# Performance work log

Measured on AMD Instinct MI355X. Metric: run time of the kernel, lower is better.

## Reference

```python
import jax, jax.numpy as jnp
import numpy as np

GAMMA = 1.0

def setup_inputs() -> dict:
    key = jax.random.key(0)
    k1, k2 = jax.random.split(key)
    source_features = jax.random.normal(k1, (4096, 2048), dtype=jnp.float32)
    target_features = jax.random.normal(k2, (4096, 2048), dtype=jnp.float32)
    return {"source_features": source_features, "target_features": target_features}

def _gaussian_kernel_mean(x, y, gamma):
    # Original: ((x_i - y_j)**2).mean(-1) / D  == sqdist_ij / D**2
    # Computed via the x^2 + y^2 - 2xy GEMM trick instead of tiling O(N*M*D).
    d = x.shape[1]
    x2 = jnp.sum(x * x, axis=1)  # [N]
    y2 = jnp.sum(y * y, axis=1)  # [M]
    xy = x @ y.T                 # [N, M]
    sqdist = x2[:, None] + y2[None, :] - 2.0 * xy
    k = jnp.exp(-gamma * sqdist / (d * d))
    return jnp.mean(k)

def reference(source_features, target_features):
    source = source_features.reshape(source_features.shape[0], -1)
    target = target_features.reshape(target_features.shape[0], -1)
    # Equal batch sizes -> padding branch in the original is a no-op.
    xx = _gaussian_kernel_mean(source, source, GAMMA)
    yy = _gaussian_kernel_mean(target, target, GAMMA)
    xy = _gaussian_kernel_mean(source, target, GAMMA)
    return xx + yy - 2.0 * xy
```

## Files before the change

kernel.cpp:

```cpp
#include <hip/hip_runtime.h>
#include <stdint.h>
#include <stddef.h>

#define AS1 __attribute__((address_space(1)))
#define AS3 __attribute__((address_space(3)))

typedef short bf16x8 __attribute__((ext_vector_type(8)));
typedef float f32x4 __attribute__((ext_vector_type(4)));
typedef unsigned short u16x8 __attribute__((ext_vector_type(8)));

static constexpr int N = 4096;
static constexpr int K = 2048;
static constexpr int BM = 128;
static constexpr int TILES = N / BM;
static constexpr int NBLK = TILES * TILES;

__device__ __forceinline__ unsigned short f2bf(float f) {
  union { float f; uint32_t u; } v; v.f = f;
  return (unsigned short)((v.u + 0x7FFFu + ((v.u >> 16) & 1u)) >> 16);
}

__global__ __launch_bounds__(256) void prep_kernel(
    const float* __restrict__ X, const float* __restrict__ Y,
    float* __restrict__ x2, float* __restrict__ y2,
    unsigned short* __restrict__ Xb, unsigned short* __restrict__ Yb, int wb) {
  const int row = blockIdx.x;
  const float* src = blockIdx.y ? Y : X;
  float* nrm = blockIdx.y ? y2 : x2;
  unsigned short* dst = blockIdx.y ? Yb : Xb;
  const size_t base = (size_t)row * K + threadIdx.x * 8;
  const float4 a = *(const float4*)(src + base);
  const float4 b = *(const float4*)(src + base + 4);
  double s = (double)a.x * a.x + (double)a.y * a.y + (double)a.z * a.z +
             (double)a.w * a.w + (double)b.x * b.x + (double)b.y * b.y +
             (double)b.z * b.z + (double)b.w * b.w;
  if (wb) {
    u16x8 o;
    o[0] = f2bf(a.x); o[1] = f2bf(a.y); o[2] = f2bf(a.z); o[3] = f2bf(a.w);
    o[4] = f2bf(b.x); o[5] = f2bf(b.y); o[6] = f2bf(b.z); o[7] = f2bf(b.w);
    *(u16x8*)(dst + base) = o;
  }
#pragma unroll
  for (int off = 32; off; off >>= 1) s += __shfl_down(s, off);
  __shared__ double red[4];
  if ((threadIdx.x & 63) == 0) red[threadIdx.x >> 6] = s;
  __syncthreads();
  if (threadIdx.x == 0) nrm[row] = (float)(red[0] + red[1] + red[2] + red[3]);
}


#define RB3(bb, o) ((unsigned)((bb)*32768u + (o)*16384u))
#define VM2 asm volatile("s_waitcnt vmcnt(2)" ::: "memory")
#define VM_NONE

#define STG(O, TT, BB, H)                                                      \
  do {                                                                         \
    const unsigned short* _sp = (O) ? Bpan : Apan;                             \
    const unsigned int _so =                                                   \
        ((O) ? sB : sA) + (unsigned)(H) * 262144u + (unsigned)(TT) * 64u;      \
    const unsigned int _lb = RB3(BB, O) + (unsigned)(H) * 8192u + wseg;        \
    __builtin_amdgcn_global_load_lds(                                          \
        (const AS1 unsigned int*)(_sp + _so),                                  \
        (AS3 unsigned int*)(lds + _lb), 16, 0, 0);                             \
    __builtin_amdgcn_global_load_lds(                                          \
        (const AS1 unsigned int*)(_sp + _so + 16384u),                         \
        (AS3 unsigned int*)(lds + _lb + 512u), 16, 0, 0);                      \
  } while (0)

#define PH(KS, NH, BB, VMW, ...)                                               \
  do {                                                                         \
    if constexpr ((NH) == 0) {                                                 \
      _Pragma("unroll") for (int _mi = 0; _mi < 8; ++_mi)                      \
          af[_mi] = *(const bf16x8*)(lds + RB3(BB, 0) +                        \
                                     (aoff[_mi] ^ ((KS) * 32u)));              \
    }                                                                          \
    bf16x8 _b0 = *(const bf16x8*)(lds + RB3(BB, 1) +                           \
                                  (boff[(NH) * 2] ^ ((KS) * 32u)));            \
    bf16x8 _b1 = *(const bf16x8*)(lds + RB3(BB, 1) +                           \
                                  (boff[(NH) * 2 + 1] ^ ((KS) * 32u)));        \
    __VA_ARGS__;                                                               \
    __builtin_amdgcn_s_barrier();                                              \
    __builtin_amdgcn_s_setprio(1);                                             \
    _Pragma("unroll") for (int _mi = 0; _mi < 8; ++_mi) {                      \
      acc[_mi][(NH) * 2] = __builtin_amdgcn_mfma_f32_16x16x32_bf16(            \
          af[_mi], _b0, acc[_mi][(NH) * 2], 0, 0, 0);                          \
      acc[_mi][(NH) * 2 + 1] = __builtin_amdgcn_mfma_f32_16x16x32_bf16(        \
          af[_mi], _b1, acc[_mi][(NH) * 2 + 1], 0, 0, 0);                      \
    }                                                                          \
    __builtin_amdgcn_s_setprio(0);                                             \
    VMW;                                                                       \
    __builtin_amdgcn_s_barrier();                                              \
  } while (0)

#define TILE3(T, BB)                                                           \
  do {                                                                         \
    const int _t1 = ((T) + 1 < 32) ? (T) + 1 : 31;                             \
    const int _t2 = ((T) + 2 < 32) ? (T) + 2 : 31;                             \
    PH(0, 0, BB, VM_NONE, STG(0, _t1, 1 - (BB), 1));                           \
    PH(0, 1, BB, VM_NONE, STG(1, _t1, 1 - (BB), 0));                           \
    PH(1, 0, BB, VM_NONE, STG(1, _t1, 1 - (BB), 1));                           \
    PH(1, 1, BB, VM2,     STG(0, _t2, (BB), 0));                               \
  } while (0)

__global__ __launch_bounds__(512, 2) void mmd_gemm8(
    const unsigned short* __restrict__ Xb, const unsigned short* __restrict__ Yb,
    const float* __restrict__ x2, const float* __restrict__ y2,
    double* __restrict__ partials) {
  __shared__ __align__(16) unsigned short lds[65536];

  const int bid = blockIdx.x;
  const int logical = (bid & 7) * 62 + (bid >> 3);
  int ti, tj;
  const unsigned short *Apan, *Bpan;
  const float *rn, *cn;
  double wgt;
  if (logical < 256) {
    ti = logical & 15; tj = logical >> 4;
    Apan = Xb; Bpan = Yb; rn = x2; cn = y2; wgt = -2.0;
  } else {
    const int q = logical - 256;
    const int pp = q / 120;
    int jj = q % 120;
    int rr = 0;
    while (jj >= 15 - rr) { jj -= 15 - rr; ++rr; }
    ti = rr; tj = rr + 1 + jj;
    Apan = Bpan = pp ? Yb : Xb;
    rn = cn = pp ? y2 : x2;
    wgt = 2.0;
  }
  const int i0 = ti << 8, j0 = tj << 8;

  const int tid = threadIdx.x;
  const int w = tid >> 6, l = tid & 63;
  const int wm = w >> 2, wn = w & 3;
  const int lr = l & 15, lq = l >> 4;

  const int ci = w * 128 + l;
  const int rr0 = ci >> 3;
  const int cc0 = (ci & 7) ^ (rr0 & 7);
  const unsigned int sA = (unsigned)(i0 + rr0) * (unsigned)K + (unsigned)(cc0 * 8);
  const unsigned int sB = (unsigned)(j0 + rr0) * (unsigned)K + (unsigned)(cc0 * 8);
  const unsigned int wseg = (unsigned)w * 1024u;

  unsigned int aoff[8], boff[4];
#pragma unroll
  for (int mi = 0; mi < 8; ++mi) {
    const int r = wm * 128 + mi * 16 + lr;
    aoff[mi] = (unsigned)(r * 64 + ((lq ^ (r & 7)) * 8));
  }
#pragma unroll
  for (int ni = 0; ni < 4; ++ni) {
    const int rb = wn * 64 + ni * 16 + lr;
    boff[ni] = (unsigned)(rb * 64 + ((lq ^ (rb & 7)) * 8));
  }

  f32x4 acc[8][4] = {};
  bf16x8 af[8];

  STG(0, 0, 0, 0); STG(0, 0, 0, 1); STG(1, 0, 0, 0); STG(1, 0, 0, 1);
  STG(0, 1, 1, 0);
  VM2;
  __builtin_amdgcn_s_barrier();

#pragma unroll 1
  for (int tt = 0; tt < 32; tt += 2) {
    TILE3(tt, 0);
    TILE3(tt + 1, 1);
  }

  const float ce = -1.0f / (2048.0f * 2048.0f);
  double s = 0.0;
#pragma unroll
  for (int mi = 0; mi < 8; ++mi) {
#pragma unroll
    for (int r4 = 0; r4 < 4; ++r4) {
      const float rv = rn[i0 + wm * 128 + mi * 16 + lq * 4 + r4];
#pragma unroll
      for (int ni = 0; ni < 4; ++ni) {
        const float cv = cn[j0 + wn * 64 + ni * 16 + lr];
        const float tx = ce * (rv + cv - 2.0f * acc[mi][ni][r4]);
        const float v =
            tx * (1.0f + tx * (0.5f + tx * (0.16666667f + tx * 0.041666668f)));
        s += (double)v;
      }
    }
  }
#pragma unroll
  for (int off = 32; off; off >>= 1) s += __shfl_down(s, off);
  __shared__ double red[8];
  if (l == 0) red[w] = s;
  __syncthreads();
  if (tid == 0) {
    double tot = 0.0;
#pragma unroll
    for (int i = 0; i < 8; ++i) tot += red[i];
    partials[logical] = wgt * tot;
  }
}

__global__ __launch_bounds__(256) void mmd_sym128(
    const unsigned short* __restrict__ Xb, const unsigned short* __restrict__ Yb,
    const float* __restrict__ x2, const float* __restrict__ y2,
    double* __restrict__ partials) {
  const int bid = blockIdx.x;
  const int logical = (bid & 7) * 12 + (bid >> 3);
  const int p = logical / 48;
  const int r2_ = logical % 48;
  const int d = r2_ / 3;
  const int sub = r2_ % 3;
  const double wgt = (sub == 1) ? 2.0 : 1.0;

  const unsigned short* Pan = p ? Yb : Xb;
  const float* nrm = p ? y2 : x2;
  const int i0 = d * 256 + ((sub == 2) ? 128 : 0);
  const int j0 = d * 256 + ((sub >= 1) ? 128 : 0);

  __shared__ __align__(16) unsigned short As[128 * 64];
  __shared__ __align__(16) unsigned short Bs[128 * 64];

  const int tid = threadIdx.x;
  const int w = tid >> 6, l = tid & 63;
  const int m_base = (w >> 1) * 64, n_base = (w & 1) * 64;
  const int lr = l & 15, lq = l >> 4;

  f32x4 acc[4][4] = {};

  for (int k0 = 0; k0 < K; k0 += 64) {
#pragma unroll
    for (int u = 0; u < 4; ++u) {
      const int seg = w * 4 + u;
      const int f = seg * 64 + l;
      const int row = f >> 3;
      const int scol = ((f & 7) ^ (row & 7)) * 8;
      __builtin_amdgcn_global_load_lds(
          (const AS1 unsigned int*)(Pan + (size_t)(i0 + row) * K + k0 + scol),
          (AS3 unsigned int*)(As + seg * 512), 16, 0, 0);
      __builtin_amdgcn_global_load_lds(
          (const AS1 unsigned int*)(Pan + (size_t)(j0 + row) * K + k0 + scol),
          (AS3 unsigned int*)(Bs + seg * 512), 16, 0, 0);
    }
    __syncthreads();

#pragma unroll
    for (int kk = 0; kk < 64; kk += 32) {
      bf16x8 af2[4], bfr[4];
      const int ch = (kk >> 3) + lq;
#pragma unroll
      for (int mi = 0; mi < 4; ++mi) {
        const int r = m_base + mi * 16 + lr;
        af2[mi] = *(const bf16x8*)((const char*)As + r * 128 + ((ch ^ (r & 7)) * 16));
      }
#pragma unroll
      for (int ni = 0; ni < 4; ++ni) {
        const int r = n_base + ni * 16 + lr;
        bfr[ni] = *(const bf16x8*)((const char*)Bs + r * 128 + ((ch ^ (r & 7)) * 16));
      }
#pragma unroll
      for (int mi = 0; mi < 4; ++mi)
#pragma unroll
        for (int ni = 0; ni < 4; ++ni)
          acc[mi][ni] = __builtin_amdgcn_mfma_f32_16x16x32_bf16(
              af2[mi], bfr[ni], acc[mi][ni], 0, 0, 0);
    }
    __syncthreads();
  }

  const float ce = -1.0f / (2048.0f * 2048.0f);
  double s = 0.0;
#pragma unroll
  for (int mi = 0; mi < 4; ++mi) {
#pragma unroll
    for (int r4 = 0; r4 < 4; ++r4) {
      const float rv = nrm[i0 + m_base + mi * 16 + lq * 4 + r4];
#pragma unroll
      for (int ni = 0; ni < 4; ++ni) {
        const float cv = nrm[j0 + n_base + ni * 16 + lr];
        const float tx = ce * (rv + cv - 2.0f * acc[mi][ni][r4]);
        const float v =
            tx * (1.0f + tx * (0.5f + tx * (0.16666667f + tx * 0.041666668f)));
        s += (double)v;
      }
    }
  }
#pragma unroll
  for (int off = 32; off; off >>= 1) s += __shfl_down(s, off);
  __shared__ double red[4];
  if (l == 0) red[w] = s;
  __syncthreads();
  if (tid == 0)
    partials[496 + logical] = wgt * (red[0] + red[1] + red[2] + red[3]);
}

__global__ __launch_bounds__(256) void mmd_gemm_f32(
    const float* __restrict__ Xp, const float* __restrict__ Yp,
    const float* __restrict__ x2, const float* __restrict__ y2,
    double* __restrict__ partials) {
  const int p = blockIdx.y;
  const float* Ap = (p == 1) ? Yp : Xp;
  const float* Bp = (p == 0) ? Xp : Yp;
  const float* rn = (p == 1) ? y2 : x2;
  const float* cn = (p == 0) ? x2 : y2;
  const double wgt = (p == 2) ? -2.0 : 1.0;

  const int bx = blockIdx.x;
  const int i0 = (bx & (TILES - 1)) * BM;
  const int j0 = (bx / TILES) * BM;

  __shared__ __align__(16) unsigned short As[BM * 64];
  __shared__ __align__(16) unsigned short Bs[BM * 64];

  const int tid = threadIdx.x;
  const int w = tid >> 6, l = tid & 63;
  const int m_base = (w >> 1) * 64, n_base = (w & 1) * 64;

  f32x4 acc[4][4] = {};

  for (int k0 = 0; k0 < K; k0 += 64) {
#pragma unroll
    for (int u = 0; u < 4; ++u) {
      const int f = u * 256 + tid;
      const int row = f >> 3;
      const int cir = f & 7;
      const int dstb = row * 128 + ((cir ^ (row & 7)) * 16);
      {
        const float* g = Ap + (size_t)(i0 + row) * K + k0 + cir * 8;
        const float4 v0 = *(const float4*)g;
        const float4 v1 = *(const float4*)(g + 4);
        u16x8 o;
        o[0] = f2bf(v0.x); o[1] = f2bf(v0.y); o[2] = f2bf(v0.z); o[3] = f2bf(v0.w);
        o[4] = f2bf(v1.x); o[5] = f2bf(v1.y); o[6] = f2bf(v1.z); o[7] = f2bf(v1.w);
        *(u16x8*)((char*)As + dstb) = o;
      }
      {
        const float* g = Bp + (size_t)(j0 + row) * K + k0 + cir * 8;
        const float4 v0 = *(const float4*)g;
        const float4 v1 = *(const float4*)(g + 4);
        u16x8 o;
        o[0] = f2bf(v0.x); o[1] = f2bf(v0.y); o[2] = f2bf(v0.z); o[3] = f2bf(v0.w);
        o[4] = f2bf(v1.x); o[5] = f2bf(v1.y); o[6] = f2bf(v1.z); o[7] = f2bf(v1.w);
        *(u16x8*)((char*)Bs + dstb) = o;
      }
    }
    __syncthreads();

#pragma unroll
    for (int kk = 0; kk < 64; kk += 32) {
      bf16x8 af2[4], bfr[4];
      const int lr = l & 15;
      const int ch = (kk >> 3) + (l >> 4);
#pragma unroll
      for (int mi = 0; mi < 4; ++mi) {
        const int r = m_base + mi * 16 + lr;
        af2[mi] = *(const bf16x8*)((const char*)As + r * 128 + ((ch ^ (r & 7)) * 16));
      }
#pragma unroll
      for (int ni = 0; ni < 4; ++ni) {
        const int r = n_base + ni * 16 + lr;
        bfr[ni] = *(const bf16x8*)((const char*)Bs + r * 128 + ((ch ^ (r & 7)) * 16));
      }
#pragma unroll
      for (int mi = 0; mi < 4; ++mi)
#pragma unroll
        for (int ni = 0; ni < 4; ++ni)
          acc[mi][ni] = __builtin_amdgcn_mfma_f32_16x16x32_bf16(
              af2[mi], bfr[ni], acc[mi][ni], 0, 0, 0);
    }
    __syncthreads();
  }

  const float ce = -1.0f / (2048.0f * 2048.0f);
  double s = 0.0;
  const int lr = l & 15, lq = l >> 4;
#pragma unroll
  for (int mi = 0; mi < 4; ++mi) {
#pragma unroll
    for (int r4 = 0; r4 < 4; ++r4) {
      const float rv = rn[i0 + m_base + mi * 16 + lq * 4 + r4];
#pragma unroll
      for (int ni = 0; ni < 4; ++ni) {
        const float cv = cn[j0 + n_base + ni * 16 + lr];
        const float tx = ce * (rv + cv - 2.0f * acc[mi][ni][r4]);
        const float v =
            tx * (1.0f + tx * (0.5f + tx * (0.16666667f + tx * 0.041666668f)));
        s += (double)v;
      }
    }
  }
#pragma unroll
  for (int off = 32; off; off >>= 1) s += __shfl_down(s, off);
  __shared__ double red[4];
  if (l == 0) red[w] = s;
  __syncthreads();
  if (tid == 0) partials[p * NBLK + bx] = wgt * (red[0] + red[1] + red[2] + red[3]);
}

__global__ __launch_bounds__(256) void finalize_kernel(
    const double* __restrict__ partials, float* __restrict__ out, int n) {
  double s = 0.0;
  for (int i = threadIdx.x; i < n; i += 256) s += partials[i];
#pragma unroll
  for (int off = 32; off; off >>= 1) s += __shfl_down(s, off);
  __shared__ double red[4];
  if ((threadIdx.x & 63) == 0) red[threadIdx.x >> 6] = s;
  __syncthreads();
  if (threadIdx.x == 0)
    out[0] = (float)((red[0] + red[1] + red[2] + red[3]) *
                     (1.0 / ((double)N * (double)N)));
}

extern "C" void kernel_launch(void* const* d_in, const int* in_sizes, int n_in,
                              void* d_out, int out_size, void* d_ws,
                              size_t ws_size, hipStream_t stream) {
  const float* X = (const float*)d_in[0];
  const float* Y = (const float*)d_in[1];
  char* ws = (char*)d_ws;

  double* partials = (double*)ws;
  float* x2 = (float*)(ws + 24576);
  float* y2 = (float*)(ws + 24576 + 16384);
  unsigned short* Xb = (unsigned short*)(ws + 65536);
  unsigned short* Yb = Xb + (size_t)N * K;
  const size_t need_fast = (size_t)65536 + (size_t)2 * N * K * 2;
  const bool fast = ws_size >= need_fast;

  prep_kernel<<<dim3(N, 2), 256, 0, stream>>>(X, Y, x2, y2, Xb, Yb, fast ? 1 : 0);
  if (fast) {
    mmd_gemm8<<<dim3(496), dim3(512), 0, stream>>>(Xb, Yb, x2, y2, partials);
    mmd_sym128<<<dim3(96), dim3(256), 0, stream>>>(Xb, Yb, x2, y2, partials);
    finalize_kernel<<<1, 256, 0, stream>>>(partials, (float*)d_out, 592);
  } else {
    mmd_gemm_f32<<<dim3(NBLK, 3), 256, 0, stream>>>(X, Y, x2, y2, partials);
    finalize_kernel<<<1, 256, 0, stream>>>(partials, (float*)d_out, 3072);
  }
}
```

Measured before the change: 180.1 us.

## Fold diagonal tiles into main GEMM kernel as double-work blocks, drop sym128 kernel

Removes the separate mmd_sym128 kernel that handled the diagonal 256x256 tiles with a 128-tile GEMM. The 32 diagonal tiles (16 for X·X and 16 for Y·Y) now run as the first 16 blocks of mmd_gemm8, each computing two full 256x256 tiles in sequence, and the grid grows to 512 blocks with one fewer launch. This also regroups the staging loads inside TILE3 so two loads issue in one phase and another phase issues none. The trade-off is that diagonal tiles now compute the full square instead of the upper half. The 16 double-work blocks may also lengthen the tail.

```diff
diff --git a/kernel.cpp b/kernel.cpp
--- a/kernel.cpp
+++ b/kernel.cpp
@@ -97,8 +97,8 @@
     const int _t1 = ((T) + 1 < 32) ? (T) + 1 : 31;                             \
     const int _t2 = ((T) + 2 < 32) ? (T) + 2 : 31;                             \
     PH(0, 0, BB, VM_NONE, STG(0, _t1, 1 - (BB), 1));                           \
-    PH(0, 1, BB, VM_NONE, STG(1, _t1, 1 - (BB), 0));                           \
-    PH(1, 0, BB, VM_NONE, STG(1, _t1, 1 - (BB), 1));                           \
+    PH(0, 1, BB, VM_NONE, STG(1, _t1, 1 - (BB), 0); STG(1, _t1, 1 - (BB), 1)); \
+    PH(1, 0, BB, VM_NONE, );                                                   \
     PH(1, 1, BB, VM2,     STG(0, _t2, (BB), 0));                               \
   } while (0)
 
@@ -107,28 +107,13 @@
     const float* __restrict__ x2, const float* __restrict__ y2,
     double* __restrict__ partials) {
   __shared__ __align__(16) unsigned short lds[65536];
+  __shared__ double red[8];
 
   const int bid = blockIdx.x;
-  const int logical = (bid & 7) * 62 + (bid >> 3);
-  int ti, tj;
-  const unsigned short *Apan, *Bpan;
-  const float *rn, *cn;
-  double wgt;
-  if (logical < 256) {
-    ti = logical & 15; tj = logical >> 4;
-    Apan = Xb; Bpan = Yb; rn = x2; cn = y2; wgt = -2.0;
-  } else {
-    const int q = logical - 256;
-    const int pp = q / 120;
-    int jj = q % 120;
-    int rr = 0;
-    while (jj >= 15 - rr) { jj -= 15 - rr; ++rr; }
-    ti = rr; tj = rr + 1 + jj;
-    Apan = Bpan = pp ? Yb : Xb;
-    rn = cn = pp ? y2 : x2;
-    wgt = 2.0;
-  }
-  const int i0 = ti << 8, j0 = tj << 8;
+  const bool dbl = bid < 16;
+  const int nsub = dbl ? 2 : 1;
+  int lg = 0;
+  if (!dbl) lg = ((bid - 16) & 7) * 62 + ((bid - 16) >> 3);
 
   const int tid = threadIdx.x;
   const int w = tid >> 6, l = tid & 63;
@@ -138,8 +123,6 @@
   const int ci = w * 128 + l;
   const int rr0 = ci >> 3;
   const int cc0 = (ci & 7) ^ (rr0 & 7);
-  const unsigned int sA = (unsigned)(i0 + rr0) * (unsigned)K + (unsigned)(cc0 * 8);
-  const unsigned int sB = (unsigned)(j0 + rr0) * (unsigned)K + (unsigned)(cc0 * 8);
   const unsigned int wseg = (unsigned)w * 1024u;
 
   unsigned int aoff[8], boff[4];
@@ -154,141 +137,81 @@
     boff[ni] = (unsigned)(rb * 64 + ((lq ^ (rb & 7)) * 8));
   }
 
-  f32x4 acc[8][4] = {};
-  bf16x8 af[8];
-
-  STG(0, 0, 0, 0); STG(0, 0, 0, 1); STG(1, 0, 0, 0); STG(1, 0, 0, 1);
-  STG(0, 1, 1, 0);
-  VM2;
-  __builtin_amdgcn_s_barrier();
-
 #pragma unroll 1
-  for (int tt = 0; tt < 32; tt += 2) {
-    TILE3(tt, 0);
-    TILE3(tt + 1, 1);
-  }
-
-  const float ce = -1.0f / (2048.0f * 2048.0f);
-  double s = 0.0;
-#pragma unroll
-  for (int mi = 0; mi < 8; ++mi) {
-#pragma unroll
-    for (int r4 = 0; r4 < 4; ++r4) {
-      const float rv = rn[i0 + wm * 128 + mi * 16 + lq * 4 + r4];
-#pragma unroll
-      for (int ni = 0; ni < 4; ++ni) {
-        const float cv = cn[j0 + wn * 64 + ni * 16 + lr];
-        const float tx = ce * (rv + cv - 2.0f * acc[mi][ni][r4]);
-        const float v =
-            tx * (1.0f + tx * (0.5f + tx * (0.16666667f + tx * 0.041666668f)));
-        s += (double)v;
-      }
-    }
-  }
-#pragma unroll
-  for (int off = 32; off; off >>= 1) s += __shfl_down(s, off);
-  __shared__ double red[8];
-  if (l == 0) red[w] = s;
-  __syncthreads();
-  if (tid == 0) {
-    double tot = 0.0;
-#pragma unroll
-    for (int i = 0; i < 8; ++i) tot += red[i];
-    partials[logical] = wgt * tot;
-  }
-}
-
-__global__ __launch_bounds__(256) void mmd_sym128(
-    const unsigned short* __restrict__ Xb, const unsigned short* __restrict__ Yb,
-    const float* __restrict__ x2, const float* __restrict__ y2,
-    double* __restrict__ partials) {
-  const int bid = blockIdx.x;
-  const int logical = (bid & 7) * 12 + (bid >> 3);
-  const int p = logical / 48;
-  const int r2_ = logical % 48;
-  const int d = r2_ / 3;
-  const int sub = r2_ % 3;
-  const double wgt = (sub == 1) ? 2.0 : 1.0;
-
-  const unsigned short* Pan = p ? Yb : Xb;
-  const float* nrm = p ? y2 : x2;
-  const int i0 = d * 256 + ((sub == 2) ? 128 : 0);
-  const int j0 = d * 256 + ((sub >= 1) ? 128 : 0);
-
-  __shared__ __align__(16) unsigned short As[128 * 64];
-  __shared__ __align__(16) unsigned short Bs[128 * 64];
-
-  const int tid = threadIdx.x;
-  const int w = tid >> 6, l = tid & 63;
-  const int m_base = (w >> 1) * 64, n_base = (w & 1) * 64;
-  const int lr = l & 15, lq = l >> 4;
-
-  f32x4 acc[4][4] = {};
-
-  for (int k0 = 0; k0 < K; k0 += 64) {
-#pragma unroll
-    for (int u = 0; u < 4; ++u) {
-      const int seg = w * 4 + u;
-      const int f = seg * 64 + l;
-      const int row = f >> 3;
-      const int scol = ((f & 7) ^ (row & 7)) * 8;
-      __builtin_amdgcn_global_load_lds(
-          (const AS1 unsigned int*)(Pan + (size_t)(i0 + row) * K + k0 + scol),
-          (AS3 unsigned int*)(As + seg * 512), 16, 0, 0);
-      __builtin_amdgcn_global_load_lds(
-          (const AS1 unsigned int*)(Pan + (size_t)(j0 + row) * K + k0 + scol),
-          (AS3 unsigned int*)(Bs + seg * 512), 16, 0, 0);
-    }
+  for (int sub = 0; sub < nsub; ++sub) {
+    int ti, tj, slot;
+    const unsigned short *Apan, *Bpan;
+    const float *rn, *cn;
+    double wgt;
+    if (dbl) {
+      ti = tj = bid;
+      Apan = Bpan = sub ? Yb : Xb;
+      rn = cn = sub ? y2 : x2;
+      wgt = 1.0;
+      slot = bid * 2 + sub;
+    } else if (lg < 256) {
+      ti = lg & 15; tj = lg >> 4;
+      Apan = Xb; Bpan = Yb; rn = x2; cn = y2; wgt = -2.0;
+      slot = 32 + lg;
+    } else {
+      const int q = lg - 256;
+      const int pp = q / 120;
+      int jj = q % 120;
+      int rr = 0;
+      while (jj >= 15 - rr) { jj -= 15 - rr; ++rr; }
+      ti = rr; tj = rr + 1 + jj;
+      Apan = Bpan = pp ? Yb : Xb;
+      rn = cn = pp ? y2 : x2;
+      wgt = 2.0;
+      slot = 32 + lg;
+    }
+    const int i0 = ti << 8, j0 = tj << 8;
+    const unsigned int sA = (unsigned)(i0 + rr0) * (unsigned)K + (unsigned)(cc0 * 8);
+    const unsigned int sB = (unsigned)(j0 + rr0) * (unsigned)K + (unsigned)(cc0 * 8);
+
+    f32x4 acc[8][4] = {};
+    bf16x8 af[8];
+
+    STG(0, 0, 0, 0); STG(0, 0, 0, 1); STG(1, 0, 0, 0); STG(1, 0, 0, 1);
+    STG(0, 1, 1, 0);
+    VM2;
+    __builtin_amdgcn_s_barrier();
+
+#pragma unroll 1
+    for (int tt = 0; tt < 32; tt += 2) {
+      TILE3(tt, 0);
+      TILE3(tt + 1, 1);
+    }
+
+    const float ce = -1.0f / (2048.0f * 2048.0f);
+    double s = 0.0;
+#pragma unroll
+    for (int mi = 0; mi < 8; ++mi) {
+#pragma unroll
+      for (int r4 = 0; r4 < 4; ++r4) {
+        const float rv = rn[i0 + wm * 128 + mi * 16 + lq * 4 + r4];
+#pragma unroll
+        for (int ni = 0; ni < 4; ++ni) {
+          const float cv = cn[j0 + wn * 64 + ni * 16 + lr];
+          const float tx = ce * (rv + cv - 2.0f * acc[mi][ni][r4]);
+          const float v =
+              tx * (1.0f + tx * (0.5f + tx * (0.16666667f + tx * 0.041666668f)));
+          s += (double)v;
+        }
+      }
+    }
+#pragma unroll
+    for (int off = 32; off; off >>= 1) s += __shfl_down(s, off);
+    if (l == 0) red[w] = s;
     __syncthreads();
-
-#pragma unroll
-    for (int kk = 0; kk < 64; kk += 32) {
-      bf16x8 af2[4], bfr[4];
-      const int ch = (kk >> 3) + lq;
-#pragma unroll
-      for (int mi = 0; mi < 4; ++mi) {
-        const int r = m_base + mi * 16 + lr;
-        af2[mi] = *(const bf16x8*)((const char*)As + r * 128 + ((ch ^ (r & 7)) * 16));
-      }
-#pragma unroll
-      for (int ni = 0; ni < 4; ++ni) {
-        const int r = n_base + ni * 16 + lr;
-        bfr[ni] = *(const bf16x8*)((const char*)Bs + r * 128 + ((ch ^ (r & 7)) * 16));
-      }
-#pragma unroll
-      for (int mi = 0; mi < 4; ++mi)
-#pragma unroll
-        for (int ni = 0; ni < 4; ++ni)
-          acc[mi][ni] = __builtin_amdgcn_mfma_f32_16x16x32_bf16(
-              af2[mi], bfr[ni], acc[mi][ni], 0, 0, 0);
+    if (tid == 0) {
+      double tot = 0.0;
+#pragma unroll
+      for (int i = 0; i < 8; ++i) tot += red[i];
+      partials[slot] = wgt * tot;
     }
     __syncthreads();
   }
-
-  const float ce = -1.0f / (2048.0f * 2048.0f);
-  double s = 0.0;
-#pragma unroll
-  for (int mi = 0; mi < 4; ++mi) {
-#pragma unroll
-    for (int r4 = 0; r4 < 4; ++r4) {
-      const float rv = nrm[i0 + m_base + mi * 16 + lq * 4 + r4];
-#pragma unroll
-      for (int ni = 0; ni < 4; ++ni) {
-        const float cv = nrm[j0 + n_base + ni * 16 + lr];
-        const float tx = ce * (rv + cv - 2.0f * acc[mi][ni][r4]);
-        const float v =
-            tx * (1.0f + tx * (0.5f + tx * (0.16666667f + tx * 0.041666668f)));
-        s += (double)v;
-      }
-    }
-  }
-#pragma unroll
-  for (int off = 32; off; off >>= 1) s += __shfl_down(s, off);
-  __shared__ double red[4];
-  if (l == 0) red[w] = s;
-  __syncthreads();
-  if (tid == 0)
-    partials[496 + logical] = wgt * (red[0] + red[1] + red[2] + red[3]);
 }
 
 __global__ __launch_bounds__(256) void mmd_gemm_f32(
@@ -425,9 +348,8 @@
 
   prep_kernel<<<dim3(N, 2), 256, 0, stream>>>(X, Y, x2, y2, Xb, Yb, fast ? 1 : 0);
   if (fast) {
-    mmd_gemm8<<<dim3(496), dim3(512), 0, stream>>>(Xb, Yb, x2, y2, partials);
-    mmd_sym128<<<dim3(96), dim3(256), 0, stream>>>(Xb, Yb, x2, y2, partials);
-    finalize_kernel<<<1, 256, 0, stream>>>(partials, (float*)d_out, 592);
+    mmd_gemm8<<<dim3(512), dim3(512), 0, stream>>>(Xb, Yb, x2, y2, partials);
+    finalize_kernel<<<1, 256, 0, stream>>>(partials, (float*)d_out, 528);
   } else {
     mmd_gemm_f32<<<dim3(NBLK, 3), 256, 0, stream>>>(X, Y, x2, y2, partials);
     finalize_kernel<<<1, 256, 0, stream>>>(partials, (float*)d_out, 3072);
```

After: 195.6 us. 8.6% more time.

## Prefetch LDS fragments one phase ahead and use one barrier per phase

Applied to the files above, without the earlier changes.

The GEMM main loop is software-pipelined so that the LDS reads of A and B fragments for the next phase are issued right after the current phase's MFMAs. An explicit lgkmcnt(0) wait plus a sched_barrier is placed before each MFMA group, and the second s_barrier in each phase is dropped. The goal is to hide LDS read latency behind matrix math and to halve barrier synchronization. In exchange it keeps the B fragments in extra registers. The first reads of the next buffer are also issued before the barrier, which could race with other waves' global-to-LDS loads.

```diff
diff --git a/kernel.cpp b/kernel.cpp
--- a/kernel.cpp
+++ b/kernel.cpp
@@ -51,7 +51,11 @@
 
 #define RB3(bb, o) ((unsigned)((bb)*32768u + (o)*16384u))
 #define VM2 asm volatile("s_waitcnt vmcnt(2)" ::: "memory")
-#define VM_NONE
+#define LGKM0                                                                  \
+  do {                                                                         \
+    asm volatile("s_waitcnt lgkmcnt(0)" ::: "memory");                         \
+    __builtin_amdgcn_sched_barrier(0);                                         \
+  } while (0)
 
 #define STG(O, TT, BB, H)                                                      \
   do {                                                                         \
@@ -67,39 +71,50 @@
         (AS3 unsigned int*)(lds + _lb + 512u), 16, 0, 0);                      \
   } while (0)
 
-#define PH(KS, NH, BB, VMW, ...)                                               \
+#define RDA(KS, BB)                                                            \
+  _Pragma("unroll") for (int _mi = 0; _mi < 8; ++_mi)                          \
+      af[_mi] = *(const bf16x8*)(lds + RB3(BB, 0) + (aoff[_mi] ^ ((KS) * 32u)))
+
+#define RDB(VAR, IDX, KS, BB)                                                  \
+  VAR = *(const bf16x8*)(lds + RB3(BB, 1) + (boff[IDX] ^ ((KS) * 32u)))
+
+#define MFMA_P(X0, X1, C0, C1)                                                 \
   do {                                                                         \
-    if constexpr ((NH) == 0) {                                                 \
-      _Pragma("unroll") for (int _mi = 0; _mi < 8; ++_mi)                      \
-          af[_mi] = *(const bf16x8*)(lds + RB3(BB, 0) +                        \
-                                     (aoff[_mi] ^ ((KS) * 32u)));              \
-    }                                                                          \
-    bf16x8 _b0 = *(const bf16x8*)(lds + RB3(BB, 1) +                           \
-                                  (boff[(NH) * 2] ^ ((KS) * 32u)));            \
-    bf16x8 _b1 = *(const bf16x8*)(lds + RB3(BB, 1) +                           \
-                                  (boff[(NH) * 2 + 1] ^ ((KS) * 32u)));        \
-    __VA_ARGS__;                                                               \
-    __builtin_amdgcn_s_barrier();                                              \
     __builtin_amdgcn_s_setprio(1);                                             \
     _Pragma("unroll") for (int _mi = 0; _mi < 8; ++_mi) {                      \
-      acc[_mi][(NH) * 2] = __builtin_amdgcn_mfma_f32_16x16x32_bf16(            \
-          af[_mi], _b0, acc[_mi][(NH) * 2], 0, 0, 0);                          \
-      acc[_mi][(NH) * 2 + 1] = __builtin_amdgcn_mfma_f32_16x16x32_bf16(        \
-          af[_mi], _b1, acc[_mi][(NH) * 2 + 1], 0, 0, 0);                      \
+      acc[_mi][C0] = __builtin_amdgcn_mfma_f32_16x16x32_bf16(                  \
+          af[_mi], X0, acc[_mi][C0], 0, 0, 0);                                 \
+      acc[_mi][C1] = __builtin_amdgcn_mfma_f32_16x16x32_bf16(                  \
+          af[_mi], X1, acc[_mi][C1], 0, 0, 0);                                 \
     }                                                                          \
     __builtin_amdgcn_s_setprio(0);                                             \
-    VMW;                                                                       \
-    __builtin_amdgcn_s_barrier();                                              \
   } while (0)
 
-#define TILE3(T, BB)                                                           \
+#define TILE4(T, BB)                                                           \
   do {                                                                         \
     const int _t1 = ((T) + 1 < 32) ? (T) + 1 : 31;                             \
     const int _t2 = ((T) + 2 < 32) ? (T) + 2 : 31;                             \
-    PH(0, 0, BB, VM_NONE, STG(0, _t1, 1 - (BB), 1));                           \
-    PH(0, 1, BB, VM_NONE, STG(1, _t1, 1 - (BB), 0));                           \
-    PH(1, 0, BB, VM_NONE, STG(1, _t1, 1 - (BB), 1));                           \
-    PH(1, 1, BB, VM2,     STG(0, _t2, (BB), 0));                               \
+                                                               \
+    LGKM0; MFMA_P(b0, b1, 0, 1);                                               \
+    RDB(b2, 2, 0, BB); RDB(b3, 3, 0, BB);                                      \
+    STG(0, _t1, 1 - (BB), 1);                                                  \
+    __builtin_amdgcn_s_barrier();                                              \
+                                                               \
+    LGKM0; MFMA_P(b2, b3, 2, 3);                                               \
+    RDA(1, BB); RDB(b0, 0, 1, BB); RDB(b1, 1, 1, BB);                          \
+    STG(1, _t1, 1 - (BB), 0);                                                  \
+    __builtin_amdgcn_s_barrier();                                              \
+                                                               \
+    LGKM0; MFMA_P(b0, b1, 0, 1);                                               \
+    RDB(b2, 2, 1, BB); RDB(b3, 3, 1, BB);                                      \
+    STG(1, _t1, 1 - (BB), 1);                                                  \
+    __builtin_amdgcn_s_barrier();                                              \
+                                                               \
+    LGKM0; MFMA_P(b2, b3, 2, 3);                                               \
+    STG(0, _t2, (BB), 0);                                                      \
+    VM2;                                                                       \
+    RDA(0, 1 - (BB)); RDB(b0, 0, 0, 1 - (BB)); RDB(b1, 1, 0, 1 - (BB));        \
+    __builtin_amdgcn_s_barrier();                                              \
   } while (0)
 
 __global__ __launch_bounds__(512, 2) void mmd_gemm8(
@@ -155,17 +170,18 @@
   }
 
   f32x4 acc[8][4] = {};
-  bf16x8 af[8];
+  bf16x8 af[8], b0, b1, b2, b3;
 
   STG(0, 0, 0, 0); STG(0, 0, 0, 1); STG(1, 0, 0, 0); STG(1, 0, 0, 1);
   STG(0, 1, 1, 0);
   VM2;
   __builtin_amdgcn_s_barrier();
+  RDA(0, 0); RDB(b0, 0, 0, 0); RDB(b1, 1, 0, 0);
 
 #pragma unroll 1
   for (int tt = 0; tt < 32; tt += 2) {
-    TILE3(tt, 0);
-    TILE3(tt + 1, 1);
+    TILE4(tt, 0);
+    TILE4(tt + 1, 1);
   }
 
   const float ce = -1.0f / (2048.0f * 2048.0f);
```

New measurement: 175.0 us. 2.8% less time.
